# Optimization experiments

Hardware: AMD Instinct MI355X
Metric: run time of the kernel (lower is better)

The kernel has to match this reference:

```python
import jax, jax.numpy as jnp
import numpy as np

N_NODES = 100000
N_EDGES = 1200000
IN_F = 64
OUT_F = 64


def setup_inputs() -> dict:
    key = jax.random.key(0)
    ks = jax.random.split(key, 8)
    rows = jax.random.randint(ks[0], (N_EDGES,), 0, N_NODES)
    cols = jax.random.randint(ks[1], (N_EDGES,), 0, N_NODES)
    vals = jax.random.uniform(ks[2], (N_EDGES,), dtype=jnp.float32)
    features = jax.random.normal(ks[3], (N_NODES, IN_F), dtype=jnp.float32)
    W1 = jax.random.normal(ks[4], (IN_F, OUT_F), dtype=jnp.float32) / np.sqrt(IN_F)
    b1 = jax.random.normal(ks[5], (OUT_F,), dtype=jnp.float32) * 0.01
    W2 = jax.random.normal(ks[6], (IN_F, OUT_F), dtype=jnp.float32) / np.sqrt(IN_F)
    b2 = jax.random.normal(ks[7], (OUT_F,), dtype=jnp.float32) * 0.01
    return {"rows": rows, "cols": cols, "vals": vals, "features": features,
            "W1": W1, "b1": b1, "W2": W2, "b2": b2}


def _spmm(rows, cols, vals, x):
    # y[r] = sum_{e: rows[e]==r} vals[e] * x[cols[e]]  -- COO SpMM via gather + segment_sum
    msgs = vals[:, None] * x[cols]  # [E, F]
    return jax.ops.segment_sum(msgs, rows, num_segments=N_NODES)


def reference(rows, cols, vals, features, W1, b1, W2, b2):
    # L1 = laplacian + selfLoop(identity)  =>  L1 @ X = L @ X + X
    agg1 = _spmm(rows, cols, vals, features) + features          # [N, inF]
    inter_feature = features * features                           # elementwise square
    agg2 = _spmm(rows, cols, vals, inter_feature)                 # [N, inF]
    part1 = agg1 @ W1 + b1                                        # linear
    part2 = agg2 @ W2 + b2                                        # interActTransform
    return part1 + part2
```

## Files before the change

kernel.cpp:

```cpp
#include <hip/hip_runtime.h>


#define ROWS_PER_BUCKET 128
#define ROW_SHIFT 7
#define NBUCK_PAD 784
#define SCAN_T 196
#define CAP 2048
#define CHUNK 4096
#define EPT 16
#define MAXB 2048
#define COL_BITS 17
#define COL_MASK 0x1FFFF
#define OVF_CAP 65536

typedef __attribute__((ext_vector_type(8))) short bf16x8;
typedef __attribute__((ext_vector_type(4))) float f32x4;

__device__ __forceinline__ unsigned short f2bf(float x) {
    unsigned u = __float_as_uint(x);
    unsigned r = (u + 0x7FFFu + ((u >> 16) & 1u)) >> 16;
    return (unsigned short)r;
}
__device__ __forceinline__ float bf2f(unsigned short h) {
    return __uint_as_float(((unsigned)h) << 16);
}

__global__ __launch_bounds__(256) void cursor_init(
    int* __restrict__ gcursor, int* __restrict__ ovf_count) {
    int i = blockIdx.x * 256 + threadIdx.x;
    if (i < NBUCK_PAD) gcursor[i] = i * CAP;
    if (i == 0) *ovf_count = 0;
}

__global__ __launch_bounds__(256) void nt_scatter(
    const float* __restrict__ X, const float* __restrict__ W1,
    const float* __restrict__ b1, const float* __restrict__ W2,
    const float* __restrict__ b2, unsigned short* __restrict__ Yb,
    float* __restrict__ Z, int n_nodes, int nt_blocks,
    const int* __restrict__ rows, const int* __restrict__ cols,
    const float* __restrict__ vals, int* __restrict__ gcursor,
    int2* __restrict__ packed, int* __restrict__ ovf_count,
    int4* __restrict__ ovf, int n_edges)
{
    __shared__ int lcount[NBUCK_PAD];
    __shared__ int lstart[NBUCK_PAD];
    __shared__ int gbase[NBUCK_PAD];
    __shared__ int2 sxy[CHUNK];
    __shared__ unsigned short sbk[CHUNK];
    __shared__ int wsum[4];

    const int tid = threadIdx.x;

    if (blockIdx.x < (unsigned)nt_blocks) {
        const int lane = tid & 63;
        const int wave = tid >> 6;
        const int lg = lane >> 4;
        const int lr = lane & 15;
        const int base = blockIdx.x * 128 + wave * 32;

        bf16x8 bw1[2][4];
        bf16x8 bw2[2][4];
#pragma unroll
        for (int ks = 0; ks < 2; ++ks) {
#pragma unroll
            for (int cf = 0; cf < 4; ++cf) {
                const int col = cf * 16 + lr;
                const int k0 = ks * 32 + lg * 8;
                bf16x8 t1, t2;
#pragma unroll
                for (int j = 0; j < 8; ++j) {
                    t1[j] = (short)f2bf(W1[(k0 + j) * 64 + col]);
                    t2[j] = (short)f2bf(W2[(k0 + j) * 64 + col]);
                }
                bw1[ks][cf] = t1;
                bw2[ks][cf] = t2;
            }
        }

        f32x4 acc1[2][4];
        f32x4 acc2[2][4];
#pragma unroll
        for (int rf = 0; rf < 2; ++rf)
#pragma unroll
            for (int cf = 0; cf < 4; ++cf) {
                acc1[rf][cf] = (f32x4){0.f, 0.f, 0.f, 0.f};
                acc2[rf][cf] = (f32x4){0.f, 0.f, 0.f, 0.f};
            }

#pragma unroll
        for (int rf = 0; rf < 2; ++rf) {
            const int row = base + rf * 16 + lr;
            const bool rok = row < n_nodes;
            const float* xp = X + (size_t)row * 64 + lg * 8;
#pragma unroll
            for (int ks = 0; ks < 2; ++ks) {
                float xv[8];
                if (rok) {
                    float4 v0 = *(const float4*)(xp + ks * 32);
                    float4 v1 = *(const float4*)(xp + ks * 32 + 4);
                    xv[0] = v0.x; xv[1] = v0.y; xv[2] = v0.z; xv[3] = v0.w;
                    xv[4] = v1.x; xv[5] = v1.y; xv[6] = v1.z; xv[7] = v1.w;
                } else {
#pragma unroll
                    for (int j = 0; j < 8; ++j) xv[j] = 0.f;
                }
                bf16x8 a, q;
#pragma unroll
                for (int j = 0; j < 8; ++j) {
                    a[j] = (short)f2bf(xv[j]);
                    float s = xv[j] * xv[j];
                    q[j] = (short)f2bf(s);
                }
#pragma unroll
                for (int cf = 0; cf < 4; ++cf) {
                    acc1[rf][cf] = __builtin_amdgcn_mfma_f32_16x16x32_bf16(
                        a, bw1[ks][cf], acc1[rf][cf], 0, 0, 0);
                    acc2[rf][cf] = __builtin_amdgcn_mfma_f32_16x16x32_bf16(
                        q, bw2[ks][cf], acc2[rf][cf], 0, 0, 0);
                }
            }
        }

        float bsv[4];
#pragma unroll
        for (int cf = 0; cf < 4; ++cf)
            bsv[cf] = b1[cf * 16 + lr] + b2[cf * 16 + lr];

#pragma unroll
        for (int rf = 0; rf < 2; ++rf) {
#pragma unroll
            for (int i = 0; i < 4; ++i) {
                const int row = base + rf * 16 + lg * 4 + i;
                if (row < n_nodes) {
#pragma unroll
                    for (int cf = 0; cf < 4; ++cf) {
                        const float v1 = acc1[rf][cf][i];
                        const float y = v1 + acc2[rf][cf][i];
                        const float z = v1 + bsv[cf];
                        Yb[(size_t)row * 64 + cf * 16 + lr] = f2bf(y);
                        Z[(size_t)row * 64 + cf * 16 + lr] = z;
                    }
                }
            }
        }
        return;
    }

    int eb0 = (blockIdx.x - nt_blocks) * CHUNK;
    int cnt = min(CHUNK, n_edges - eb0);
    if (cnt <= 0) return;

    for (int k = tid; k < NBUCK_PAD; k += 256) lcount[k] = 0;
    __syncthreads();

    int eb_[EPT], ep_[EPT], ex_[EPT], ey_[EPT];
#pragma unroll
    for (int t = 0; t < EPT; ++t) {
        int i = tid + 256 * t;
        if (i < cnt) {
            int r = rows[eb0 + i];
            int b = r >> ROW_SHIFT;
            eb_[t] = b;
            ep_[t] = atomicAdd(&lcount[b], 1);
            ex_[t] = ((r & (ROWS_PER_BUCKET - 1)) << COL_BITS) | cols[eb0 + i];
            ey_[t] = __float_as_int(vals[eb0 + i]);
        } else {
            eb_[t] = -1; ep_[t] = 0; ex_[t] = 0; ey_[t] = 0;
        }
    }
    __syncthreads();

    int c0 = 0, c1 = 0, c2 = 0, c3 = 0, psum = 0;
    if (tid < SCAN_T) {
        c0 = lcount[tid * 4 + 0]; c1 = lcount[tid * 4 + 1];
        c2 = lcount[tid * 4 + 2]; c3 = lcount[tid * 4 + 3];
        psum = c0 + c1 + c2 + c3;
    }
    const int lane = tid & 63;
    const int wv = tid >> 6;
    int incl = psum;
#pragma unroll
    for (int o = 1; o < 64; o <<= 1) {
        int n = __shfl_up(incl, o);
        if (lane >= o) incl += n;
    }
    if (lane == 63) wsum[wv] = incl;
    __syncthreads();
    int wpre = 0;
#pragma unroll
    for (int w = 0; w < 3; ++w)
        if (w < wv) wpre += wsum[w];
    int base0 = wpre + incl - psum;
    if (tid < SCAN_T) {
        lstart[tid * 4 + 0] = base0;
        lstart[tid * 4 + 1] = base0 + c0;
        lstart[tid * 4 + 2] = base0 + c0 + c1;
        lstart[tid * 4 + 3] = base0 + c0 + c1 + c2;
    }
    __syncthreads();

    for (int k = tid; k < NBUCK_PAD; k += 256) {
        if (lcount[k] > 0) gbase[k] = atomicAdd(&gcursor[k], lcount[k]);
    }

#pragma unroll
    for (int t = 0; t < EPT; ++t) {
        if (eb_[t] >= 0) {
            int p = lstart[eb_[t]] + ep_[t];
            sxy[p] = make_int2(ex_[t], ey_[t]);
            sbk[p] = (unsigned short)eb_[t];
        }
    }
    __syncthreads();

    for (int i = tid; i < cnt; i += 256) {
        int b = sbk[i];
        int2 a = sxy[i];
        int dest = gbase[b] + (i - lstart[b]);
        if (dest < (b + 1) * CAP) {
            packed[dest] = a;
        } else {
            int p = atomicAdd(ovf_count, 1);
            if (p < OVF_CAP)
                ovf[p] = make_int4(b * ROWS_PER_BUCKET + (a.x >> COL_BITS),
                                   a.x & COL_MASK, a.y, 0);
        }
    }
}

__global__ __launch_bounds__(256) void bucket_gather_quads(
    const int* __restrict__ gcursor, const int2* __restrict__ packed,
    const unsigned short* __restrict__ Yb, float* __restrict__ out,
    int n_nodes) {
    __shared__ int2 sxy[MAXB];
    __shared__ int hist[ROWS_PER_BUCKET];
    __shared__ int chs[ROWS_PER_BUCKET];
    __shared__ int chc[ROWS_PER_BUCKET];

    int tid = threadIdx.x;
    int bucket = blockIdx.x >> 1;
    int rhalf = (blockIdx.x & 1) * 64;
    int fquad = tid & 15;
    int grp = tid >> 4;
    int s = bucket * CAP;
    int e = min(gcursor[bucket], s + CAP);
    int row0 = bucket * ROWS_PER_BUCKET;
    const uint2* __restrict__ Y64 = (const uint2*)Yb;

    for (int cb = s; cb < e; cb += MAXB) {
        int cnt = min(MAXB, e - cb);

        if (tid < ROWS_PER_BUCKET) hist[tid] = 0;
        __syncthreads();

        for (int i = tid; i < cnt; i += 256)
            atomicAdd(&hist[packed[cb + i].x >> COL_BITS], 1);
        __syncthreads();

        if (tid < ROWS_PER_BUCKET) chs[tid] = hist[tid];
        __syncthreads();
#pragma unroll
        for (int o = 1; o < ROWS_PER_BUCKET; o <<= 1) {
            int t = 0;
            if (tid < ROWS_PER_BUCKET && tid >= o) t = chs[tid - o];
            __syncthreads();
            if (tid < ROWS_PER_BUCKET) chs[tid] += t;
            __syncthreads();
        }
        if (tid < ROWS_PER_BUCKET) {
            int excl = chs[tid] - hist[tid];
            chs[tid] = excl;
            chc[tid] = excl;
        }
        __syncthreads();

        for (int i = tid; i < cnt; i += 256) {
            int2 a = packed[cb + i];
            int p = atomicAdd(&chc[a.x >> COL_BITS], 1);
            sxy[p] = a;
        }
        __syncthreads();

        for (int rr = 0; rr < 4; ++rr) {
            int r = rhalf + grp * 4 + rr;
            int rc = hist[r];
            int node = row0 + r;
            if (rc == 0 || node >= n_nodes) continue;
            int rs = chs[r];
            float a0 = 0.f, a1 = 0.f, a2 = 0.f, a3 = 0.f;
            int j = 0;
            for (; j + 4 <= rc; j += 4) {
                int2 e0 = sxy[rs + j + 0], e1 = sxy[rs + j + 1];
                int2 e2 = sxy[rs + j + 2], e3 = sxy[rs + j + 3];
                uint2 u0 = Y64[(size_t)(e0.x & COL_MASK) * 16 + fquad];
                uint2 u1 = Y64[(size_t)(e1.x & COL_MASK) * 16 + fquad];
                uint2 u2 = Y64[(size_t)(e2.x & COL_MASK) * 16 + fquad];
                uint2 u3 = Y64[(size_t)(e3.x & COL_MASK) * 16 + fquad];
                float v0 = __int_as_float(e0.y), v1 = __int_as_float(e1.y);
                float v2 = __int_as_float(e2.y), v3 = __int_as_float(e3.y);
                a0 = fmaf(v0, __uint_as_float(u0.x << 16), a0);
                a1 = fmaf(v0, __uint_as_float(u0.x & 0xFFFF0000u), a1);
                a2 = fmaf(v0, __uint_as_float(u0.y << 16), a2);
                a3 = fmaf(v0, __uint_as_float(u0.y & 0xFFFF0000u), a3);
                a0 = fmaf(v1, __uint_as_float(u1.x << 16), a0);
                a1 = fmaf(v1, __uint_as_float(u1.x & 0xFFFF0000u), a1);
                a2 = fmaf(v1, __uint_as_float(u1.y << 16), a2);
                a3 = fmaf(v1, __uint_as_float(u1.y & 0xFFFF0000u), a3);
                a0 = fmaf(v2, __uint_as_float(u2.x << 16), a0);
                a1 = fmaf(v2, __uint_as_float(u2.x & 0xFFFF0000u), a1);
                a2 = fmaf(v2, __uint_as_float(u2.y << 16), a2);
                a3 = fmaf(v2, __uint_as_float(u2.y & 0xFFFF0000u), a3);
                a0 = fmaf(v3, __uint_as_float(u3.x << 16), a0);
                a1 = fmaf(v3, __uint_as_float(u3.x & 0xFFFF0000u), a1);
                a2 = fmaf(v3, __uint_as_float(u3.y << 16), a2);
                a3 = fmaf(v3, __uint_as_float(u3.y & 0xFFFF0000u), a3);
            }
            for (; j < rc; ++j) {
                int2 e0 = sxy[rs + j];
                uint2 u0 = Y64[(size_t)(e0.x & COL_MASK) * 16 + fquad];
                float v0 = __int_as_float(e0.y);
                a0 = fmaf(v0, __uint_as_float(u0.x << 16), a0);
                a1 = fmaf(v0, __uint_as_float(u0.x & 0xFFFF0000u), a1);
                a2 = fmaf(v0, __uint_as_float(u0.y << 16), a2);
                a3 = fmaf(v0, __uint_as_float(u0.y & 0xFFFF0000u), a3);
            }
            float4* op = (float4*)(out + (size_t)node * 64 + fquad * 4);
            float4 o = *op;
            o.x += a0; o.y += a1; o.z += a2; o.w += a3;
            *op = o;
        }
        __syncthreads();
    }
}

__global__ __launch_bounds__(256) void overflow_scatter(
    const int* __restrict__ ovf_count, const int4* __restrict__ ovf,
    const unsigned short* __restrict__ Yb, float* __restrict__ out) {
    int cnt = min(*ovf_count, OVF_CAP);
    long long total = (long long)cnt * 64;
    for (long long i = blockIdx.x * 256 + threadIdx.x; i < total;
         i += (long long)gridDim.x * 256) {
        int e = (int)(i >> 6), f = (int)(i & 63);
        int4 a = ovf[e];
        atomicAdd(&out[(size_t)a.x * 64 + f],
                  __int_as_float(a.z) * bf2f(Yb[(size_t)a.y * 64 + f]));
    }
}


__global__ __launch_bounds__(256) void edge_scatter(
    const int* __restrict__ rows, const int* __restrict__ cols,
    const float* __restrict__ vals, const unsigned short* __restrict__ Yb,
    float* __restrict__ out, int n_edges)
{
    int t = blockIdx.x * 256 + threadIdx.x;
    int e = t >> 4;
    int f = (t & 15) << 2;
    if (e >= n_edges) return;
    int r = rows[e];
    int c = cols[e];
    float v = vals[e];
    const unsigned short* y = Yb + (size_t)c * 64 + f;
    float* o = out + (size_t)r * 64 + f;
    atomicAdd(o + 0, v * bf2f(y[0]));
    atomicAdd(o + 1, v * bf2f(y[1]));
    atomicAdd(o + 2, v * bf2f(y[2]));
    atomicAdd(o + 3, v * bf2f(y[3]));
}

extern "C" void kernel_launch(void* const* d_in, const int* in_sizes, int n_in,
                              void* d_out, int out_size, void* d_ws, size_t ws_size,
                              hipStream_t stream) {
    const int*   rows = (const int*)d_in[0];
    const int*   cols = (const int*)d_in[1];
    const float* vals = (const float*)d_in[2];
    const float* X    = (const float*)d_in[3];
    const float* W1   = (const float*)d_in[4];
    const float* b1   = (const float*)d_in[5];
    const float* W2   = (const float*)d_in[6];
    const float* b2   = (const float*)d_in[7];
    float* out = (float*)d_out;

    const int n_edges = in_sizes[0];
    const int n_nodes = in_sizes[3] / 64;
    const int nbuck = (n_nodes + ROWS_PER_BUCKET - 1) / ROWS_PER_BUCKET;

    char* ws = (char*)d_ws;
    size_t o_Yb     = 0;
    size_t o_packed = o_Yb + (size_t)n_nodes * 64 * 2;
    size_t o_ovf    = o_packed + (size_t)NBUCK_PAD * CAP * 8;
    size_t o_gcurs  = o_ovf + (size_t)OVF_CAP * 16;
    size_t o_ovfcnt = o_gcurs + NBUCK_PAD * 4;
    size_t need     = o_ovfcnt + 16;

    unsigned short* Yb = (unsigned short*)(ws + o_Yb);

    const bool fastpath =
        ws_size >= need && nbuck <= NBUCK_PAD && n_nodes <= (1 << COL_BITS);

    int2* packed  = (int2*)(ws + o_packed);
    int4* ovf     = (int4*)(ws + o_ovf);
    int*  gcursor = (int*)(ws + o_gcurs);
    int*  ovfcnt  = (int*)(ws + o_ovfcnt);

    int nblocks = (n_nodes + 127) / 128;

    if (fastpath) {
        int eb = (n_edges + CHUNK - 1) / CHUNK;
        cursor_init<<<(NBUCK_PAD + 255) / 256, 256, 0, stream>>>(gcursor, ovfcnt);
        nt_scatter<<<nblocks + eb, 256, 0, stream>>>(
            X, W1, b1, W2, b2, Yb, out, n_nodes, nblocks,
            rows, cols, vals, gcursor, packed, ovfcnt, ovf, n_edges);
        bucket_gather_quads<<<nbuck * 2, 256, 0, stream>>>(gcursor, packed, Yb,
                                                           out, n_nodes);
        overflow_scatter<<<128, 256, 0, stream>>>(ovfcnt, ovf, Yb, out);
    } else {
        nt_scatter<<<nblocks, 256, 0, stream>>>(
            X, W1, b1, W2, b2, Yb, out, n_nodes, nblocks,
            rows, cols, vals, (int*)0, (int2*)0, (int*)0, (int4*)0, 0);
        long long threads = (long long)n_edges * 16;
        int eblocks = (int)((threads + 255) / 256);
        edge_scatter<<<eblocks, 256, 0, stream>>>(rows, cols, vals, Yb, out, n_edges);
    }
}
```

Before: 162.4 us.

## Interleave GEMM and scatter blocks; one 512-thread block per bucket with shuffle scan

The fused launch now interleaves node-transform blocks with edge-scatter blocks through a proportional mapping, so both kinds of work run side by side across the grid instead of all GEMM blocks being scheduled first. The bucket gather kernel now uses one 512-thread block per bucket instead of two 256-thread blocks that each repeated the histogram, scan and shared-memory sort. This removes that duplicated bucket preprocessing and replaces the barrier-heavy shared-memory scan with wavefront shuffles. The trade-offs are fewer, larger blocks in the gather stage and a __syncthreads call inside divergent branches, which every thread still reaches.

```diff
diff --git a/kernel.cpp b/kernel.cpp
--- a/kernel.cpp
+++ b/kernel.cpp
@@ -8,7 +8,6 @@
 #define CAP 2048
 #define CHUNK 4096
 #define EPT 16
-#define MAXB 2048
 #define COL_BITS 17
 #define COL_MASK 0x1FFFF
 #define OVF_CAP 65536
@@ -36,7 +35,7 @@
     const float* __restrict__ X, const float* __restrict__ W1,
     const float* __restrict__ b1, const float* __restrict__ W2,
     const float* __restrict__ b2, unsigned short* __restrict__ Yb,
-    float* __restrict__ Z, int n_nodes, int nt_blocks,
+    float* __restrict__ Z, int n_nodes, int nt_blocks, int eb_blocks,
     const int* __restrict__ rows, const int* __restrict__ cols,
     const float* __restrict__ vals, int* __restrict__ gcursor,
     int2* __restrict__ packed, int* __restrict__ ovf_count,
@@ -50,13 +49,18 @@
     __shared__ int wsum[4];
 
     const int tid = threadIdx.x;
-
-    if (blockIdx.x < (unsigned)nt_blocks) {
+    const int g = blockIdx.x;
+    const int total = nt_blocks + eb_blocks;
+    const int lo = (int)(((long long)g * eb_blocks) / total);
+    const int hi = (int)(((long long)(g + 1) * eb_blocks) / total);
+
+    if (hi == lo) {
+        const int ntb = g - lo;
         const int lane = tid & 63;
         const int wave = tid >> 6;
         const int lg = lane >> 4;
         const int lr = lane & 15;
-        const int base = blockIdx.x * 128 + wave * 32;
+        const int base = ntb * 128 + wave * 32;
 
         bf16x8 bw1[2][4];
         bf16x8 bw2[2][4];
@@ -146,7 +150,7 @@
         return;
     }
 
-    int eb0 = (blockIdx.x - nt_blocks) * CHUNK;
+    int eb0 = lo * CHUNK;
     int cnt = min(CHUNK, n_edges - eb0);
     if (cnt <= 0) return;
 
@@ -228,108 +232,106 @@
     }
 }
 
-__global__ __launch_bounds__(256) void bucket_gather_quads(
+__global__ __launch_bounds__(512) void bucket_gather_full(
     const int* __restrict__ gcursor, const int2* __restrict__ packed,
     const unsigned short* __restrict__ Yb, float* __restrict__ out,
     int n_nodes) {
-    __shared__ int2 sxy[MAXB];
+    __shared__ int2 sxy[CAP];
     __shared__ int hist[ROWS_PER_BUCKET];
     __shared__ int chs[ROWS_PER_BUCKET];
     __shared__ int chc[ROWS_PER_BUCKET];
+    __shared__ int w0sum;
 
     int tid = threadIdx.x;
-    int bucket = blockIdx.x >> 1;
-    int rhalf = (blockIdx.x & 1) * 64;
+    int bucket = blockIdx.x;
     int fquad = tid & 15;
     int grp = tid >> 4;
     int s = bucket * CAP;
     int e = min(gcursor[bucket], s + CAP);
+    int cnt = e - s;
     int row0 = bucket * ROWS_PER_BUCKET;
     const uint2* __restrict__ Y64 = (const uint2*)Yb;
 
-    for (int cb = s; cb < e; cb += MAXB) {
-        int cnt = min(MAXB, e - cb);
-
-        if (tid < ROWS_PER_BUCKET) hist[tid] = 0;
+    if (tid < ROWS_PER_BUCKET) hist[tid] = 0;
+    __syncthreads();
+
+    for (int i = tid; i < cnt; i += 512)
+        atomicAdd(&hist[packed[s + i].x >> COL_BITS], 1);
+    __syncthreads();
+
+    if (tid < ROWS_PER_BUCKET) {
+        int h = hist[tid];
+        int incl = h;
+        const int lane = tid & 63;
+#pragma unroll
+        for (int o = 1; o < 64; o <<= 1) {
+            int n = __shfl_up(incl, o);
+            if (lane >= o) incl += n;
+        }
+        if (tid == 63) w0sum = incl;
         __syncthreads();
-
-        for (int i = tid; i < cnt; i += 256)
-            atomicAdd(&hist[packed[cb + i].x >> COL_BITS], 1);
+        int excl = incl - h + (tid >= 64 ? w0sum : 0);
+        chs[tid] = excl;
+        chc[tid] = excl;
+    } else {
         __syncthreads();
-
-        if (tid < ROWS_PER_BUCKET) chs[tid] = hist[tid];
-        __syncthreads();
-#pragma unroll
-        for (int o = 1; o < ROWS_PER_BUCKET; o <<= 1) {
-            int t = 0;
-            if (tid < ROWS_PER_BUCKET && tid >= o) t = chs[tid - o];
-            __syncthreads();
-            if (tid < ROWS_PER_BUCKET) chs[tid] += t;
-            __syncthreads();
-        }
-        if (tid < ROWS_PER_BUCKET) {
-            int excl = chs[tid] - hist[tid];
-            chs[tid] = excl;
-            chc[tid] = excl;
-        }
-        __syncthreads();
-
-        for (int i = tid; i < cnt; i += 256) {
-            int2 a = packed[cb + i];
-            int p = atomicAdd(&chc[a.x >> COL_BITS], 1);
-            sxy[p] = a;
-        }
-        __syncthreads();
-
-        for (int rr = 0; rr < 4; ++rr) {
-            int r = rhalf + grp * 4 + rr;
-            int rc = hist[r];
-            int node = row0 + r;
-            if (rc == 0 || node >= n_nodes) continue;
-            int rs = chs[r];
-            float a0 = 0.f, a1 = 0.f, a2 = 0.f, a3 = 0.f;
-            int j = 0;
-            for (; j + 4 <= rc; j += 4) {
-                int2 e0 = sxy[rs + j + 0], e1 = sxy[rs + j + 1];
-                int2 e2 = sxy[rs + j + 2], e3 = sxy[rs + j + 3];
-                uint2 u0 = Y64[(size_t)(e0.x & COL_MASK) * 16 + fquad];
-                uint2 u1 = Y64[(size_t)(e1.x & COL_MASK) * 16 + fquad];
-                uint2 u2 = Y64[(size_t)(e2.x & COL_MASK) * 16 + fquad];
-                uint2 u3 = Y64[(size_t)(e3.x & COL_MASK) * 16 + fquad];
-                float v0 = __int_as_float(e0.y), v1 = __int_as_float(e1.y);
-                float v2 = __int_as_float(e2.y), v3 = __int_as_float(e3.y);
-                a0 = fmaf(v0, __uint_as_float(u0.x << 16), a0);
-                a1 = fmaf(v0, __uint_as_float(u0.x & 0xFFFF0000u), a1);
-                a2 = fmaf(v0, __uint_as_float(u0.y << 16), a2);
-                a3 = fmaf(v0, __uint_as_float(u0.y & 0xFFFF0000u), a3);
-                a0 = fmaf(v1, __uint_as_float(u1.x << 16), a0);
-                a1 = fmaf(v1, __uint_as_float(u1.x & 0xFFFF0000u), a1);
-                a2 = fmaf(v1, __uint_as_float(u1.y << 16), a2);
-                a3 = fmaf(v1, __uint_as_float(u1.y & 0xFFFF0000u), a3);
-                a0 = fmaf(v2, __uint_as_float(u2.x << 16), a0);
-                a1 = fmaf(v2, __uint_as_float(u2.x & 0xFFFF0000u), a1);
-                a2 = fmaf(v2, __uint_as_float(u2.y << 16), a2);
-                a3 = fmaf(v2, __uint_as_float(u2.y & 0xFFFF0000u), a3);
-                a0 = fmaf(v3, __uint_as_float(u3.x << 16), a0);
-                a1 = fmaf(v3, __uint_as_float(u3.x & 0xFFFF0000u), a1);
-                a2 = fmaf(v3, __uint_as_float(u3.y << 16), a2);
-                a3 = fmaf(v3, __uint_as_float(u3.y & 0xFFFF0000u), a3);
-            }
-            for (; j < rc; ++j) {
-                int2 e0 = sxy[rs + j];
-                uint2 u0 = Y64[(size_t)(e0.x & COL_MASK) * 16 + fquad];
-                float v0 = __int_as_float(e0.y);
-                a0 = fmaf(v0, __uint_as_float(u0.x << 16), a0);
-                a1 = fmaf(v0, __uint_as_float(u0.x & 0xFFFF0000u), a1);
-                a2 = fmaf(v0, __uint_as_float(u0.y << 16), a2);
-                a3 = fmaf(v0, __uint_as_float(u0.y & 0xFFFF0000u), a3);
-            }
-            float4* op = (float4*)(out + (size_t)node * 64 + fquad * 4);
-            float4 o = *op;
-            o.x += a0; o.y += a1; o.z += a2; o.w += a3;
-            *op = o;
-        }
-        __syncthreads();
+    }
+    __syncthreads();
+
+    for (int i = tid; i < cnt; i += 512) {
+        int2 a = packed[s + i];
+        int p = atomicAdd(&chc[a.x >> COL_BITS], 1);
+        sxy[p] = a;
+    }
+    __syncthreads();
+
+    for (int rr = 0; rr < 4; ++rr) {
+        int r = grp * 4 + rr;
+        int rc = hist[r];
+        int node = row0 + r;
+        if (rc == 0 || node >= n_nodes) continue;
+        int rs = chs[r];
+        float a0 = 0.f, a1 = 0.f, a2 = 0.f, a3 = 0.f;
+        int j = 0;
+        for (; j + 4 <= rc; j += 4) {
+            int2 e0 = sxy[rs + j + 0], e1 = sxy[rs + j + 1];
+            int2 e2 = sxy[rs + j + 2], e3 = sxy[rs + j + 3];
+            uint2 u0 = Y64[(size_t)(e0.x & COL_MASK) * 16 + fquad];
+            uint2 u1 = Y64[(size_t)(e1.x & COL_MASK) * 16 + fquad];
+            uint2 u2 = Y64[(size_t)(e2.x & COL_MASK) * 16 + fquad];
+            uint2 u3 = Y64[(size_t)(e3.x & COL_MASK) * 16 + fquad];
+            float v0 = __int_as_float(e0.y), v1 = __int_as_float(e1.y);
+            float v2 = __int_as_float(e2.y), v3 = __int_as_float(e3.y);
+            a0 = fmaf(v0, __uint_as_float(u0.x << 16), a0);
+            a1 = fmaf(v0, __uint_as_float(u0.x & 0xFFFF0000u), a1);
+            a2 = fmaf(v0, __uint_as_float(u0.y << 16), a2);
+            a3 = fmaf(v0, __uint_as_float(u0.y & 0xFFFF0000u), a3);
+            a0 = fmaf(v1, __uint_as_float(u1.x << 16), a0);
+            a1 = fmaf(v1, __uint_as_float(u1.x & 0xFFFF0000u), a1);
+            a2 = fmaf(v1, __uint_as_float(u1.y << 16), a2);
+            a3 = fmaf(v1, __uint_as_float(u1.y & 0xFFFF0000u), a3);
+            a0 = fmaf(v2, __uint_as_float(u2.x << 16), a0);
+            a1 = fmaf(v2, __uint_as_float(u2.x & 0xFFFF0000u), a1);
+            a2 = fmaf(v2, __uint_as_float(u2.y << 16), a2);
+            a3 = fmaf(v2, __uint_as_float(u2.y & 0xFFFF0000u), a3);
+            a0 = fmaf(v3, __uint_as_float(u3.x << 16), a0);
+            a1 = fmaf(v3, __uint_as_float(u3.x & 0xFFFF0000u), a1);
+            a2 = fmaf(v3, __uint_as_float(u3.y << 16), a2);
+            a3 = fmaf(v3, __uint_as_float(u3.y & 0xFFFF0000u), a3);
+        }
+        for (; j < rc; ++j) {
+            int2 e0 = sxy[rs + j];
+            uint2 u0 = Y64[(size_t)(e0.x & COL_MASK) * 16 + fquad];
+            float v0 = __int_as_float(e0.y);
+            a0 = fmaf(v0, __uint_as_float(u0.x << 16), a0);
+            a1 = fmaf(v0, __uint_as_float(u0.x & 0xFFFF0000u), a1);
+            a2 = fmaf(v0, __uint_as_float(u0.y << 16), a2);
+            a3 = fmaf(v0, __uint_as_float(u0.y & 0xFFFF0000u), a3);
+        }
+        float4* op = (float4*)(out + (size_t)node * 64 + fquad * 4);
+        float4 o = *op;
+        o.x += a0; o.y += a1; o.z += a2; o.w += a3;
+        *op = o;
     }
 }
 
@@ -409,14 +411,14 @@
         int eb = (n_edges + CHUNK - 1) / CHUNK;
         cursor_init<<<(NBUCK_PAD + 255) / 256, 256, 0, stream>>>(gcursor, ovfcnt);
         nt_scatter<<<nblocks + eb, 256, 0, stream>>>(
-            X, W1, b1, W2, b2, Yb, out, n_nodes, nblocks,
+            X, W1, b1, W2, b2, Yb, out, n_nodes, nblocks, eb,
             rows, cols, vals, gcursor, packed, ovfcnt, ovf, n_edges);
-        bucket_gather_quads<<<nbuck * 2, 256, 0, stream>>>(gcursor, packed, Yb,
-                                                           out, n_nodes);
+        bucket_gather_full<<<nbuck, 512, 0, stream>>>(gcursor, packed, Yb,
+                                                      out, n_nodes);
         overflow_scatter<<<128, 256, 0, stream>>>(ovfcnt, ovf, Yb, out);
     } else {
         nt_scatter<<<nblocks, 256, 0, stream>>>(
-            X, W1, b1, W2, b2, Yb, out, n_nodes, nblocks,
+            X, W1, b1, W2, b2, Yb, out, n_nodes, nblocks, 0,
             rows, cols, vals, (int*)0, (int2*)0, (int*)0, (int4*)0, 0);
         long long threads = (long long)n_edges * 16;
         int eblocks = (int)((threads + 255) / 256);
```

After: 165.6 us. +2.0%, slower.
